# Kernel tuning notes

Hardware: AMD Instinct MI355X
Metric: run time of the kernel (lower is better)

## Reference

```python
import jax, jax.numpy as jnp
import numpy as np

D_MODEL = 768
N_HEADS = 12
D_K = D_MODEL // N_HEADS
SCALE = 1.0 / np.sqrt(D_K).astype(np.float32)


def setup_inputs() -> dict:
    key = jax.random.key(0)
    ks = jax.random.split(key, 11)
    B, S, D = 2, 2048, D_MODEL
    std = 1.0 / np.sqrt(D).astype(np.float32)
    x = jax.random.normal(ks[0], (B, S, D), dtype=jnp.float32)
    def lin(kw, kb):
        W = jax.random.normal(kw, (D, D), dtype=jnp.float32) * std
        b = jax.random.normal(kb, (D,), dtype=jnp.float32) * std
        return W, b
    Wq, bq = lin(ks[1], ks[2])
    Wk, bk = lin(ks[3], ks[4])
    Wv, bv = lin(ks[5], ks[6])
    Wo, bo = lin(ks[7], ks[8])   # linear_w_out
    Wf, bf = lin(ks[9], ks[10])  # linear_final_layer
    return {"x": x, "Wq": Wq, "bq": bq, "Wk": Wk, "bk": bk, "Wv": Wv,
            "bv": bv, "Wo": Wo, "bo": bo, "Wf": Wf, "bf": bf}


def reference(x, Wq, bq, Wk, bk, Wv, bv, Wo, bo, Wf, bf):
    B, S, D = x.shape
    H, dk = N_HEADS, D_K
    # torch Linear: y = x @ W.T + b
    q = (x @ Wq.T + bq).reshape(B, H, S, dk)  # faithful: view, NOT transpose-split
    k = (x @ Wk.T + bk).reshape(B, H, S, dk)
    v = (x @ Wv.T + bv).reshape(B, H, S, dk)
    # scores = q @ k^T  -> [B,H,S,S]
    scores = jnp.einsum('bhsd,bhtd->bhst', q, k)
    # faithful quirk: softmax AFTER (scores/sqrt(dk)) @ v, over d_k axis
    attn = jax.nn.softmax(jnp.einsum('bhst,bhtd->bhsd', scores * SCALE, v), axis=-1)
    multi_head = attn.reshape(B, S, D)
    multi_head = multi_head @ Wo.T + bo
    out = multi_head @ Wf.T + bf
    return out
```

## Files before the change

kernel.cpp:

```cpp
#include <hip/hip_runtime.h>
#include <math.h>

typedef unsigned short u16;
typedef unsigned int   u32;
typedef __attribute__((ext_vector_type(8))) _Float16 f16x8;
typedef __attribute__((ext_vector_type(4))) float f32x4;

#define DMODEL 768
#define SEQ    2048
#define BATCH  2
#define NHEAD  12
#define DKH    64
#define PER_BATCH (SEQ*DMODEL)
#define PER_HEAD  (SEQ*DKH)
#define ATT_SCALE 0.125f

__device__ inline u16 f2h(float f) {
    _Float16 h = (_Float16)f;
    return *(u16*)&h;
}
__device__ inline float4 h4f(uint2 v) {
    _Float16* p = (_Float16*)&v;
    return make_float4((float)p[0], (float)p[1], (float)p[2], (float)p[3]);
}

__device__ inline void async_load16(const void* g, void* l) {
    __builtin_amdgcn_global_load_lds(
        (const __attribute__((address_space(1))) unsigned int*)g,
        (__attribute__((address_space(3))) unsigned int*)l, 16, 0, 0);
}

__global__ void conv_all(const float* __restrict__ x,
                         const float* __restrict__ Wq, const float* __restrict__ Wk,
                         const float* __restrict__ Wv, const float* __restrict__ Wf,
                         const float* __restrict__ Wo,
                         const float* __restrict__ bo, const float* __restrict__ bfb,
                         u16* xh, u16* Wh3, u16* Wfh, u16* WoT, float* bc)
{
    const int z = blockIdx.y;
    if (z == 5) {
        if (blockIdx.x >= 48) return;
        const int row    = blockIdx.x * 16 + (threadIdx.x >> 4);
        const int lane16 = threadIdx.x & 15;
        const float* r = Wf + (size_t)row * 768;
        float s = 0.f;
        #pragma unroll
        for (int t = 0; t < 48; ++t) s += r[lane16 + 16 * t] * bo[lane16 + 16 * t];
        #pragma unroll
        for (int off = 8; off > 0; off >>= 1) s += __shfl_xor(s, off, 64);
        if (lane16 == 0) bc[row] = s + bfb[row];
        return;
    }
    if (z == 6) {
        __shared__ u16 S[32][33];
        const int bi = blockIdx.x / 24, bj = blockIdx.x % 24;
        const int r  = threadIdx.x >> 3;
        const int c4 = threadIdx.x & 7;
        float4 v = *(const float4*)&Wo[(size_t)(bi * 32 + r) * 768 + bj * 32 + c4 * 4];
        S[c4 * 4 + 0][r] = f2h(v.x); S[c4 * 4 + 1][r] = f2h(v.y);
        S[c4 * 4 + 2][r] = f2h(v.z); S[c4 * 4 + 3][r] = f2h(v.w);
        __syncthreads();
        u16 o0 = S[r][c4 * 4 + 0], o1 = S[r][c4 * 4 + 1];
        u16 o2 = S[r][c4 * 4 + 2], o3 = S[r][c4 * 4 + 3];
        uint2 pk; pk.x = (u32)o0 | ((u32)o1 << 16); pk.y = (u32)o2 | ((u32)o3 << 16);
        *(uint2*)&WoT[(size_t)(bj * 32 + r) * 768 + bi * 32 + c4 * 4] = pk;
        return;
    }
    const float* src; u16* dst; int n;
    switch (z) {
        case 0: src = x;  dst = xh;            n = 3145728; break;
        case 1: src = Wq; dst = Wh3;           n = 589824;  break;
        case 2: src = Wk; dst = Wh3 + 589824;  n = 589824;  break;
        case 3: src = Wv; dst = Wh3 + 1179648; n = 589824;  break;
        default:src = Wf; dst = Wfh;           n = 589824;  break;
    }
    const int n4 = n >> 2;
    for (int i = blockIdx.x * blockDim.x + threadIdx.x; i < n4; i += gridDim.x * blockDim.x) {
        float4 v = ((const float4*)src)[i];
        u16 h0 = f2h(v.x), h1 = f2h(v.y), h2 = f2h(v.z), h3 = f2h(v.w);
        uint2 hp; hp.x = (u32)h0 | ((u32)h1 << 16); hp.y = (u32)h2 | ((u32)h3 << 16);
        ((uint2*)dst)[i] = hp;
    }
}

__global__ __launch_bounds__(256, 3) void qkv_gemm(
    const u16* __restrict__ xh, const u16* __restrict__ Wh3,
    const u16* __restrict__ Wfh, const u16* __restrict__ WoT,
    const float* __restrict__ bq, const float* __restrict__ bk, const float* __restrict__ bv,
    float* __restrict__ Q, u16* __restrict__ Kh, u16* __restrict__ Vh,
    u16* __restrict__ Wcb)
{
    const int tid = threadIdx.x;
    const int w   = tid >> 6;
    const int L   = tid & 63;
    const int wr  = w >> 1, wc = w & 1;

    const u16 *Ap, *Bp;
    int mBase, nBaseB, mode;
    if (blockIdx.y == 18) {
        if (blockIdx.x >= 36) return;
        Ap = Wfh; Bp = WoT;
        mBase  = (blockIdx.x / 6) * 128;
        nBaseB = (blockIdx.x % 6) * 128;
        mode = 3;
    } else {
        if (blockIdx.x >= 32) return;
        Ap = xh; Bp = Wh3;
        mBase  = blockIdx.x * 128;
        nBaseB = blockIdx.y * 128;
        mode = nBaseB / 768;
    }

    __shared__ __align__(16) u16 As[128 * 64];
    __shared__ __align__(16) u16 Bs[128 * 64];

    f32x4 acc[4][4];
    #pragma unroll
    for (int i = 0; i < 4; ++i)
        #pragma unroll
        for (int j = 0; j < 4; ++j)
            acc[i][j] = (f32x4){0.f, 0.f, 0.f, 0.f};

    const int srow = L >> 3;
    const int kScr = ((L & 7) ^ (srow & 7)) * 8;
    const int rin = L & 15, q = L >> 4;

    for (int kb = 0; kb < 768; kb += 64) {
        if (kb) __syncthreads();
        #pragma unroll
        for (int cc = 0; cc < 2; ++cc) {
            const int ch = w * 2 + cc;
            const size_t rA = (size_t)(mBase + ch * 16 + srow) * 768 + kb + kScr;
            async_load16(&Ap[rA],           &As[ch * 1024]);
            async_load16(&Ap[rA + 8 * 768], &As[ch * 1024 + 512]);
            const size_t rB = (size_t)(nBaseB + ch * 16 + srow) * 768 + kb + kScr;
            async_load16(&Bp[rB],           &Bs[ch * 1024]);
            async_load16(&Bp[rB + 8 * 768], &Bs[ch * 1024 + 512]);
        }
        __syncthreads();

        #pragma unroll
        for (int kq = 0; kq < 2; ++kq) {
            const int slot = ((kq * 4 + q) ^ (rin & 7)) * 8;
            f16x8 af[4], bfr[4];
            #pragma unroll
            for (int i = 0; i < 4; ++i)
                af[i] = *(const f16x8*)&As[(wr * 64 + i * 16 + rin) * 64 + slot];
            #pragma unroll
            for (int j = 0; j < 4; ++j)
                bfr[j] = *(const f16x8*)&Bs[(wc * 64 + j * 16 + rin) * 64 + slot];
            #pragma unroll
            for (int i = 0; i < 4; ++i)
                #pragma unroll
                for (int j = 0; j < 4; ++j)
                    acc[i][j] = __builtin_amdgcn_mfma_f32_16x16x32_f16(af[i], bfr[j], acc[i][j], 0, 0, 0);
        }
    }

    const int nOff = (mode == 3) ? nBaseB : (nBaseB % 768);
    const float* bias = (mode == 0) ? bq : ((mode == 1) ? bk : ((mode == 2) ? bv : nullptr));
    u16* Ch = (mode == 1) ? Kh : ((mode == 2) ? Vh : Wcb);

    #pragma unroll
    for (int j = 0; j < 4; ++j) {
        const int c = nOff + wc * 64 + j * 16 + rin;
        const float bvl = bias ? bias[c] : 0.f;
        #pragma unroll
        for (int i = 0; i < 4; ++i) {
            const int r0 = mBase + wr * 64 + i * 16 + q * 4;
            #pragma unroll
            for (int reg = 0; reg < 4; ++reg) {
                const float v = acc[i][j][reg] + bvl;
                if (mode == 0) Q[(size_t)(r0 + reg) * 768 + c] = v;
                else           Ch[(size_t)(r0 + reg) * 768 + c] = f2h(v);
            }
        }
    }
}

__global__ __launch_bounds__(256, 4) void gemm_f16(
    const u16* __restrict__ A, const u16* __restrict__ B,
    const float* __restrict__ bias, float* __restrict__ C)
{
    const int tid = threadIdx.x;
    const int w   = tid >> 6;
    const int L   = tid & 63;
    const int wr  = w >> 1, wc = w & 1;
    const int mBase = blockIdx.x * 64;
    const int nBase = blockIdx.y * 128;

    __shared__ __align__(16) u16 As[64 * 64];
    __shared__ __align__(16) u16 Bs[128 * 64];

    f32x4 acc[2][4];
    #pragma unroll
    for (int i = 0; i < 2; ++i)
        #pragma unroll
        for (int j = 0; j < 4; ++j)
            acc[i][j] = (f32x4){0.f, 0.f, 0.f, 0.f};

    const int srow = L >> 3;
    const int kScr = ((L & 7) ^ (srow & 7)) * 8;
    const int rin = L & 15, q = L >> 4;

    for (int kb = 0; kb < 768; kb += 64) {
        if (kb) __syncthreads();
        {
            const size_t rA = (size_t)(mBase + w * 16 + srow) * 768 + kb + kScr;
            async_load16(&A[rA],           &As[w * 1024]);
            async_load16(&A[rA + 8 * 768], &As[w * 1024 + 512]);
        }
        #pragma unroll
        for (int cc = 0; cc < 2; ++cc) {
            const int cB = w * 2 + cc;
            const size_t rB = (size_t)(nBase + cB * 16 + srow) * 768 + kb + kScr;
            async_load16(&B[rB],           &Bs[cB * 1024]);
            async_load16(&B[rB + 8 * 768], &Bs[cB * 1024 + 512]);
        }
        __syncthreads();

        #pragma unroll
        for (int kq = 0; kq < 2; ++kq) {
            const int slot = ((kq * 4 + q) ^ (rin & 7)) * 8;
            f16x8 af[2], bfr[4];
            #pragma unroll
            for (int i = 0; i < 2; ++i)
                af[i] = *(const f16x8*)&As[(wr * 2 + i) * 1024 + rin * 64 + slot];
            #pragma unroll
            for (int j = 0; j < 4; ++j)
                bfr[j] = *(const f16x8*)&Bs[(wc * 4 + j) * 1024 + rin * 64 + slot];
            #pragma unroll
            for (int i = 0; i < 2; ++i)
                #pragma unroll
                for (int j = 0; j < 4; ++j)
                    acc[i][j] = __builtin_amdgcn_mfma_f32_16x16x32_f16(af[i], bfr[j], acc[i][j], 0, 0, 0);
        }
    }

    #pragma unroll
    for (int j = 0; j < 4; ++j) {
        const int c = nBase + wc * 64 + j * 16 + rin;
        const float bvl = bias[c];
        #pragma unroll
        for (int i = 0; i < 2; ++i) {
            const int r0 = mBase + wr * 32 + i * 16 + q * 4;
            #pragma unroll
            for (int reg = 0; reg < 4; ++reg)
                C[(size_t)(r0 + reg) * 768 + c] = acc[i][j][reg] + bvl;
        }
    }
}

__global__ __launch_bounds__(256, 2) void kv_outer(
    const u16* __restrict__ Kh, const u16* __restrict__ Vh,
    float* __restrict__ Mpart)
{
    const int chunk = blockIdx.x;
    const int p     = blockIdx.y;
    const int b = p / NHEAD, h = p % NHEAD;
    const u16* Kb = Kh + (size_t)b * PER_BATCH + (size_t)h * PER_HEAD + (size_t)chunk * 128 * DKH;
    const u16* Vb = Vh + (size_t)b * PER_BATCH + (size_t)h * PER_HEAD + (size_t)chunk * 128 * DKH;

    __shared__ __align__(16) float Ks[32][64];
    __shared__ __align__(16) float Vs[32][64];

    const int tid = threadIdx.x;
    const int tx  = tid & 15;
    const int ty  = tid >> 4;

    float acc[4][4];
    #pragma unroll
    for (int i = 0; i < 4; ++i)
        #pragma unroll
        for (int j = 0; j < 4; ++j) acc[i][j] = 0.f;

    for (int t0 = 0; t0 < 128; t0 += 32) {
        if (t0) __syncthreads();
        #pragma unroll
        for (int r = 0; r < 2; ++r) {
            int idx = tid + 256 * r;
            int row = idx >> 4;
            int c4  = idx & 15;
            uint2 kp = *(const uint2*)&Kb[(size_t)(t0 + row) * DKH + c4 * 4];
            uint2 vp = *(const uint2*)&Vb[(size_t)(t0 + row) * DKH + c4 * 4];
            *(float4*)&Ks[row][c4 * 4] = h4f(kp);
            *(float4*)&Vs[row][c4 * 4] = h4f(vp);
        }
        __syncthreads();
        #pragma unroll
        for (int tt = 0; tt < 32; ++tt) {
            float4 ka = *(const float4*)&Ks[tt][ty * 4];
            float4 va = *(const float4*)&Vs[tt][tx * 4];
            float a[4] = {ka.x, ka.y, ka.z, ka.w};
            float v[4] = {va.x, va.y, va.z, va.w};
            #pragma unroll
            for (int i = 0; i < 4; ++i)
                #pragma unroll
                for (int j = 0; j < 4; ++j)
                    acc[i][j] += a[i] * v[j];
        }
    }

    float* Mo = Mpart + ((size_t)p * 16 + chunk) * 4096;
    #pragma unroll
    for (int i = 0; i < 4; ++i)
        #pragma unroll
        for (int j = 0; j < 4; ++j)
            Mo[(ty * 4 + i) * 64 + tx * 4 + j] = acc[i][j];
}

__global__ __launch_bounds__(256, 2) void reduce_M(
    const float* __restrict__ Mpart, float* __restrict__ Mred)
{
    const int p = blockIdx.x;
    const int e4 = blockIdx.y * 256 + threadIdx.x;
    const float4* Mp4 = (const float4*)Mpart + (size_t)p * 16384;
    float4 s = Mp4[e4];
    #pragma unroll
    for (int c = 1; c < 16; ++c) {
        float4 t = Mp4[(size_t)c * 1024 + e4];
        s.x += t.x; s.y += t.y; s.z += t.z; s.w += t.w;
    }
    s.x *= ATT_SCALE; s.y *= ATT_SCALE; s.z *= ATT_SCALE; s.w *= ATT_SCALE;
    ((float4*)Mred)[(size_t)p * 1024 + e4] = s;
}

__global__ __launch_bounds__(256, 2) void attn_gemm(
    const float* __restrict__ Qbuf, const float* __restrict__ Mred,
    u16* __restrict__ MH)
{
    const int chunk = blockIdx.x;
    const int p     = blockIdx.y;
    const int b = p / NHEAD, h = p % NHEAD;
    const float* Qb = Qbuf + (size_t)b * PER_BATCH + (size_t)h * PER_HEAD + (size_t)chunk * 64 * DKH;
    u16* MHb        = MH   + (size_t)b * PER_BATCH + (size_t)h * PER_HEAD + (size_t)chunk * 64 * DKH;

    __shared__ float QsT[64][65];
    __shared__ __align__(16) float SM[64][64];

    const int tid = threadIdx.x;

    const float4* M4 = (const float4*)(Mred + (size_t)p * 4096);
    float4* SM4 = (float4*)SM;
    #pragma unroll
    for (int r = 0; r < 4; ++r) {
        int e4 = tid + 256 * r;
        SM4[e4] = M4[e4];
        int row = e4 >> 4, c4 = e4 & 15;
        float4 v = *(const float4*)&Qb[(size_t)row * DKH + c4 * 4];
        QsT[c4 * 4 + 0][row] = v.x; QsT[c4 * 4 + 1][row] = v.y;
        QsT[c4 * 4 + 2][row] = v.z; QsT[c4 * 4 + 3][row] = v.w;
    }
    __syncthreads();

    const int tx = tid & 15;
    const int ty = tid >> 4;

    float acc[4][4];
    #pragma unroll
    for (int i = 0; i < 4; ++i)
        #pragma unroll
        for (int j = 0; j < 4; ++j) acc[i][j] = 0.f;

    #pragma unroll 4
    for (int k = 0; k < 64; ++k) {
        float4 bv = *(const float4*)&SM[k][tx * 4];
        float aa[4] = {QsT[k][ty * 4 + 0], QsT[k][ty * 4 + 1],
                       QsT[k][ty * 4 + 2], QsT[k][ty * 4 + 3]};
        float bb[4] = {bv.x, bv.y, bv.z, bv.w};
        #pragma unroll
        for (int i = 0; i < 4; ++i)
            #pragma unroll
            for (int j = 0; j < 4; ++j)
                acc[i][j] += aa[i] * bb[j];
    }

    #pragma unroll
    for (int i = 0; i < 4; ++i) {
        float m = fmaxf(fmaxf(acc[i][0], acc[i][1]), fmaxf(acc[i][2], acc[i][3]));
        #pragma unroll
        for (int off = 1; off < 16; off <<= 1)
            m = fmaxf(m, __shfl_xor(m, off, 64));
        float e0 = __expf(acc[i][0] - m), e1 = __expf(acc[i][1] - m);
        float e2 = __expf(acc[i][2] - m), e3 = __expf(acc[i][3] - m);
        float s = (e0 + e1) + (e2 + e3);
        #pragma unroll
        for (int off = 1; off < 16; off <<= 1)
            s += __shfl_xor(s, off, 64);
        float inv = 1.f / s;
        u16 o0 = f2h(e0 * inv), o1 = f2h(e1 * inv);
        u16 o2 = f2h(e2 * inv), o3 = f2h(e3 * inv);
        uint2 pk; pk.x = (u32)o0 | ((u32)o1 << 16); pk.y = (u32)o2 | ((u32)o3 << 16);
        const int row = ty * 4 + i;
        *(uint2*)&MHb[(size_t)row * DKH + tx * 4] = pk;
    }
}

extern "C" void kernel_launch(void* const* d_in, const int* in_sizes, int n_in,
                              void* d_out, int out_size, void* d_ws, size_t ws_size,
                              hipStream_t stream)
{
    const float* x  = (const float*)d_in[0];
    const float* Wq = (const float*)d_in[1];
    const float* bq = (const float*)d_in[2];
    const float* Wk = (const float*)d_in[3];
    const float* bk = (const float*)d_in[4];
    const float* Wv = (const float*)d_in[5];
    const float* bv = (const float*)d_in[6];
    const float* Wo = (const float*)d_in[7];
    const float* bo = (const float*)d_in[8];
    const float* Wf = (const float*)d_in[9];
    const float* bf = (const float*)d_in[10];
    float* out = (float*)d_out;

    float* ws_f = (float*)d_ws;
    float* Q   = ws_f;
    float* Mp  = ws_f + 3145728;
    float* Mrd = ws_f + 4718592;
    float* bc  = ws_f + 4816896;
    u16* ub  = (u16*)(ws_f + 4817920);
    u16* xh  = ub;
    u16* Wh3 = ub + 3145728;
    u16* Wfh = Wh3 + 1769472;
    u16* WoT = Wfh + 589824;
    u16* Wcb = WoT + 589824;
    u16* Kh  = Wcb + 589824;
    u16* Vh  = Kh  + 3145728;
    u16* MH  = xh;

    dim3 blk(256);
    conv_all<<<dim3(576, 7), blk, 0, stream>>>(x, Wq, Wk, Wv, Wf, Wo, bo, bf,
                                               xh, Wh3, Wfh, WoT, bc);
    qkv_gemm<<<dim3(36, 19), blk, 0, stream>>>(xh, Wh3, Wfh, WoT, bq, bk, bv,
                                               Q, Kh, Vh, Wcb);
    kv_outer<<<dim3(16, 24), blk, 0, stream>>>(Kh, Vh, Mp);
    reduce_M<<<dim3(24, 4), blk, 0, stream>>>(Mp, Mrd);
    attn_gemm<<<dim3(32, 24), blk, 0, stream>>>(Q, Mrd, MH);
    gemm_f16<<<dim3(64, 6), blk, 0, stream>>>(MH, Wcb, bc, out);
}
```

Measured before the change: 150.4 us.

## Fuse K^T·V partial reduction into kv kernel via last-block atomic counter

```diff
diff --git a/kernel.cpp b/kernel.cpp
--- a/kernel.cpp
+++ b/kernel.cpp
@@ -35,11 +35,16 @@
                          const float* __restrict__ Wv, const float* __restrict__ Wf,
                          const float* __restrict__ Wo,
                          const float* __restrict__ bo, const float* __restrict__ bfb,
-                         u16* xh, u16* Wh3, u16* Wfh, u16* WoT, float* bc)
+                         u16* xh, u16* Wh3, u16* Wfh, u16* WoT, float* bc,
+                         int* cnt)
 {
     const int z = blockIdx.y;
     if (z == 5) {
-        if (blockIdx.x >= 48) return;
+        if (blockIdx.x == 48) {
+            if (threadIdx.x < 32) cnt[threadIdx.x] = 0;
+            return;
+        }
+        if (blockIdx.x > 48) return;
         const int row    = blockIdx.x * 16 + (threadIdx.x >> 4);
         const int lane16 = threadIdx.x & 15;
         const float* r = Wf + (size_t)row * 768;
@@ -251,18 +256,19 @@
     }
 }
 
-__global__ __launch_bounds__(256, 2) void kv_outer(
+__global__ __launch_bounds__(256, 2) void kv_fused(
     const u16* __restrict__ Kh, const u16* __restrict__ Vh,
-    float* __restrict__ Mpart)
+    float* __restrict__ Mpart, float* __restrict__ Mred, int* __restrict__ cnt)
 {
     const int chunk = blockIdx.x;
     const int p     = blockIdx.y;
     const int b = p / NHEAD, h = p % NHEAD;
-    const u16* Kb = Kh + (size_t)b * PER_BATCH + (size_t)h * PER_HEAD + (size_t)chunk * 128 * DKH;
-    const u16* Vb = Vh + (size_t)b * PER_BATCH + (size_t)h * PER_HEAD + (size_t)chunk * 128 * DKH;
+    const u16* Kb = Kh + (size_t)b * PER_BATCH + (size_t)h * PER_HEAD + (size_t)chunk * 64 * DKH;
+    const u16* Vb = Vh + (size_t)b * PER_BATCH + (size_t)h * PER_HEAD + (size_t)chunk * 64 * DKH;
 
     __shared__ __align__(16) float Ks[32][64];
     __shared__ __align__(16) float Vs[32][64];
+    __shared__ int lastFlag;
 
     const int tid = threadIdx.x;
     const int tx  = tid & 15;
@@ -274,7 +280,7 @@
         #pragma unroll
         for (int j = 0; j < 4; ++j) acc[i][j] = 0.f;
 
-    for (int t0 = 0; t0 < 128; t0 += 32) {
+    for (int t0 = 0; t0 < 64; t0 += 32) {
         if (t0) __syncthreads();
         #pragma unroll
         for (int r = 0; r < 2; ++r) {
@@ -301,28 +307,36 @@
         }
     }
 
-    float* Mo = Mpart + ((size_t)p * 16 + chunk) * 4096;
+    float* Mo = Mpart + ((size_t)p * 32 + chunk) * 4096;
     #pragma unroll
     for (int i = 0; i < 4; ++i)
         #pragma unroll
         for (int j = 0; j < 4; ++j)
             Mo[(ty * 4 + i) * 64 + tx * 4 + j] = acc[i][j];
-}
-
-__global__ __launch_bounds__(256, 2) void reduce_M(
-    const float* __restrict__ Mpart, float* __restrict__ Mred)
-{
-    const int p = blockIdx.x;
-    const int e4 = blockIdx.y * 256 + threadIdx.x;
-    const float4* Mp4 = (const float4*)Mpart + (size_t)p * 16384;
-    float4 s = Mp4[e4];
-    #pragma unroll
-    for (int c = 1; c < 16; ++c) {
-        float4 t = Mp4[(size_t)c * 1024 + e4];
-        s.x += t.x; s.y += t.y; s.z += t.z; s.w += t.w;
-    }
-    s.x *= ATT_SCALE; s.y *= ATT_SCALE; s.z *= ATT_SCALE; s.w *= ATT_SCALE;
-    ((float4*)Mred)[(size_t)p * 1024 + e4] = s;
+
+    __threadfence();
+    __syncthreads();
+    if (tid == 0) {
+        int t = atomicAdd(&cnt[p], 1);
+        lastFlag = (t == 31);
+    }
+    __syncthreads();
+    if (!lastFlag) return;
+
+    __threadfence();
+    const float4* Mp4 = (const float4*)Mpart + (size_t)p * 32 * 1024;
+    float4* Mr4 = (float4*)Mred + (size_t)p * 1024;
+    #pragma unroll
+    for (int r = 0; r < 4; ++r) {
+        const int e4 = tid + 256 * r;
+        float4 s = Mp4[e4];
+        for (int c = 1; c < 32; ++c) {
+            float4 t = Mp4[(size_t)c * 1024 + e4];
+            s.x += t.x; s.y += t.y; s.z += t.z; s.w += t.w;
+        }
+        s.x *= ATT_SCALE; s.y *= ATT_SCALE; s.z *= ATT_SCALE; s.w *= ATT_SCALE;
+        Mr4[e4] = s;
+    }
 }
 
 __global__ __launch_bounds__(256, 2) void attn_gemm(
@@ -416,9 +430,10 @@
     float* ws_f = (float*)d_ws;
     float* Q   = ws_f;
     float* Mp  = ws_f + 3145728;
-    float* Mrd = ws_f + 4718592;
-    float* bc  = ws_f + 4816896;
-    u16* ub  = (u16*)(ws_f + 4817920);
+    float* Mrd = ws_f + 6291456;
+    float* bc  = ws_f + 6389760;
+    int*   cnt = (int*)(ws_f + 6390784);
+    u16* ub  = (u16*)(ws_f + 6391040);
     u16* xh  = ub;
     u16* Wh3 = ub + 3145728;
     u16* Wfh = Wh3 + 1769472;
@@ -430,11 +445,10 @@
 
     dim3 blk(256);
     conv_all<<<dim3(576, 7), blk, 0, stream>>>(x, Wq, Wk, Wv, Wf, Wo, bo, bf,
-                                               xh, Wh3, Wfh, WoT, bc);
+                                               xh, Wh3, Wfh, WoT, bc, cnt);
     qkv_gemm<<<dim3(36, 19), blk, 0, stream>>>(xh, Wh3, Wfh, WoT, bq, bk, bv,
                                                Q, Kh, Vh, Wcb);
-    kv_outer<<<dim3(16, 24), blk, 0, stream>>>(Kh, Vh, Mp);
-    reduce_M<<<dim3(24, 4), blk, 0, stream>>>(Mp, Mrd);
+    kv_fused<<<dim3(32, 24), blk, 0, stream>>>(Kh, Vh, Mp, Mrd, cnt);
     attn_gemm<<<dim3(32, 24), blk, 0, stream>>>(Q, Mrd, MH);
     gemm_f16<<<dim3(64, 6), blk, 0, stream>>>(MH, Wcb, bc, out);
 }
```

New measurement: 245.2 us. 63.0% more time.
